# Optimization experiments

Hardware: AMD Instinct MI355X
Metric: run time of the kernel (lower is better)

The kernel has to match this reference:

```python
import jax, jax.numpy as jnp
import numpy as np

B, T = 4, 8
H, W = 120, 160
NON_SEM = 4
CAT = 16
MAP_CH = NON_SEM + CAT          # 20 map channels
FEAT_CH = 2 * NON_SEM + CAT     # 24 feature channels
RES = 5.0                       # cm per map cell
GLOBAL_M, LOCAL_M = 960, 240    # map_size/resolution, and /downscale
M2 = LOCAL_M * LOCAL_M
HFOV = 79.0
CAM_H_CM = 88.0
VISION_CM = 100 * RES           # vision_range cells -> cm
AGENT_R2 = 2.0 ** 2
EXPLORE_R2 = 3.0 ** 2
FX = W / (2.0 * float(np.tan(np.deg2rad(HFOV) / 2.0)))
FY = FX
CX, CY = W / 2.0, H / 2.0

LOCAL_POSE0 = jnp.array([LOCAL_M * RES / 2, LOCAL_M * RES / 2, 0.0], jnp.float32)
GLOBAL_POSE0 = jnp.array([GLOBAL_M * RES / 2, GLOBAL_M * RES / 2, 0.0], jnp.float32)
OFF = (GLOBAL_M - LOCAL_M) // 2
BOUNDS0 = jnp.array([OFF, OFF + LOCAL_M, OFF, OFF + LOCAL_M], jnp.int32)
ORIGINS0 = jnp.array([OFF * RES, OFF * RES, 0.0], jnp.float32)


def _splat1(flat, w):  # scatter-add scalar weights into the flattened local grid
    return jnp.zeros((M2,), jnp.float32).at[flat].add(w)


def _splatC(flat, vals):  # vals [C, N] -> [C, M2]
    return jnp.zeros((vals.shape[0], M2), jnp.float32).at[:, flat].add(vals)


def _step(carry, xs):
    lmap, gmap, lpose, gpose, bounds, origins = carry
    obs, delta, cam_T, done, upd = xs
    doneb = done != 0
    # per-env reset on episode end (init_map_and_pose_for_env)
    lmap = jnp.where(doneb[:, None, None, None], 0.0, lmap)
    gmap = jnp.where(doneb[:, None, None, None], 0.0, gmap)
    lpose = jnp.where(doneb[:, None], LOCAL_POSE0, lpose)
    gpose = jnp.where(doneb[:, None], GLOBAL_POSE0, gpose)
    bounds = jnp.where(doneb[:, None], BOUNDS0, bounds)
    origins = jnp.where(doneb[:, None], ORIGINS0, origins)

    # dead-reckoning pose update (delta in agent frame)
    th = jnp.deg2rad(lpose[:, 2])
    dx = delta[:, 0] * jnp.cos(th) - delta[:, 1] * jnp.sin(th)
    dy = delta[:, 0] * jnp.sin(th) + delta[:, 1] * jnp.cos(th)
    lpose = lpose + jnp.stack([dx, dy, delta[:, 2]], -1)

    # depth -> camera-frame point cloud (cm)
    depth = obs[:, 3] * 400.0 + 50.0  # [B,H,W]
    sem = obs[:, NON_SEM:]            # [B,CAT,H,W]
    uu = (jnp.arange(W, dtype=jnp.float32) - CX)[None, None, :]
    vv = (CY - jnp.arange(H, dtype=jnp.float32))[None, :, None]
    pts = jnp.stack([uu * depth / FX, vv * depth / FY, depth, jnp.ones_like(depth)], -1)
    pts = jnp.einsum('bij,bhwj->bhwi', cam_T, pts)  # camera extrinsics
    x_f, y_l, z_u = pts[..., 2], -pts[..., 0], pts[..., 1] + CAM_H_CM

    # agent frame -> local map frame
    th2 = jnp.deg2rad(lpose[:, 2])[:, None, None]
    wx = lpose[:, 0][:, None, None] + x_f * jnp.cos(th2) - y_l * jnp.sin(th2)
    wy = lpose[:, 1][:, None, None] + x_f * jnp.sin(th2) + y_l * jnp.cos(th2)
    ix = jnp.floor(wx / RES).astype(jnp.int32)
    iy = jnp.floor(wy / RES).astype(jnp.int32)
    valid = (depth > 25.0) & (depth < VISION_CM) & (ix >= 0) & (ix < LOCAL_M) & (iy >= 0) & (iy < LOCAL_M)
    flat = (jnp.clip(iy, 0, LOCAL_M - 1) * LOCAL_M + jnp.clip(ix, 0, LOCAL_M - 1)).reshape(B, -1)
    vm = valid.reshape(B, -1).astype(jnp.float32)
    obst_w = vm * ((z_u > 25.0) & (z_u < 150.0)).reshape(B, -1).astype(jnp.float32)

    exp_grid = jax.vmap(_splat1)(flat, vm).reshape(B, LOCAL_M, LOCAL_M)
    obst_grid = jax.vmap(_splat1)(flat, obst_w).reshape(B, LOCAL_M, LOCAL_M)
    sem_grid = jax.vmap(_splatC)(flat, sem.reshape(B, CAT, -1) * vm[:, None, :]).reshape(B, CAT, LOCAL_M, LOCAL_M)

    # agent location / been-close disks
    g = jnp.arange(LOCAL_M, dtype=jnp.float32)
    dxg = g[None, None, :] - (lpose[:, 0] / RES)[:, None, None]
    dyg = g[None, :, None] - (lpose[:, 1] / RES)[:, None, None]
    d2 = dxg * dxg + dyg * dyg
    agent = (d2 <= AGENT_R2).astype(jnp.float32)
    close = (d2 <= EXPLORE_R2).astype(jnp.float32)

    lmap = jnp.concatenate([
        jnp.maximum(lmap[:, 0], jnp.clip(obst_grid, 0.0, 1.0))[:, None],
        jnp.maximum(lmap[:, 1], jnp.clip(exp_grid, 0.0, 1.0))[:, None],
        agent[:, None],
        jnp.maximum(lmap[:, 3], close)[:, None],
        jnp.maximum(lmap[:, NON_SEM:], jnp.clip(sem_grid, 0.0, 1.0)),
    ], axis=1)

    # fuse local window into global map for envs flagged for update
    y1, x1 = bounds[:, 0], bounds[:, 2]
    crop = jax.vmap(lambda gm, y, x: jax.lax.dynamic_slice(gm, (0, y, x), (MAP_CH, LOCAL_M, LOCAL_M)))(gmap, y1, x1)
    updb = (upd != 0)[:, None, None, None]
    fused = jnp.where(updb, jnp.maximum(crop, lmap), crop)
    gmap = jax.vmap(lambda gm, c, y, x: jax.lax.dynamic_update_slice(gm, c, (0, y, x)))(gmap, fused, y1, x1)
    gpose = jnp.where((upd != 0)[:, None], lpose + origins, gpose)

    feats = jnp.concatenate([lmap[:, :NON_SEM], fused[:, :NON_SEM], lmap[:, NON_SEM:]], axis=1)
    return (lmap, gmap, lpose, gpose, bounds, origins), (feats, lpose, gpose, bounds, origins)


def _forward(obs_seq, pose_delta, cam_poses, init_local_map, init_global_map,
             init_local_pose, init_global_pose, init_origins,
             done_flags, update_flags, init_bounds):
    xs = (obs_seq.swapaxes(0, 1), pose_delta.swapaxes(0, 1), cam_poses.swapaxes(0, 1),
          done_flags.swapaxes(0, 1), update_flags.swapaxes(0, 1))
    carry0 = (init_local_map, init_global_map, init_local_pose, init_global_pose, init_bounds, init_origins)
    carry, ys = jax.lax.scan(_step, carry0, xs)
    feats, lp, gp, bnds, orgs = ys
    return (feats.swapaxes(0, 1), carry[0], carry[1], lp.swapaxes(0, 1), gp.swapaxes(0, 1),
            bnds.swapaxes(0, 1), orgs.swapaxes(0, 1))


def setup_inputs() -> dict:
    key = jax.random.key(0)
    ks = jax.random.split(key, 5)
    obs_seq = jax.random.uniform(ks[0], (B, T, MAP_CH, H, W), jnp.float32)
    pose_delta = jax.random.normal(ks[1], (B, T, 3), jnp.float32) * jnp.array([10.0, 2.0, 5.0], jnp.float32)
    cam_poses = jnp.eye(4, dtype=jnp.float32)[None, None] + 0.02 * jax.random.normal(ks[2], (B, T, 4, 4), jnp.float32)
    done_flags = jax.random.randint(ks[3], (B, T), 0, 2, jnp.int32)
    update_flags = jax.random.randint(ks[4], (B, T), 0, 2, jnp.int32)
    return {
        'obs_seq': obs_seq,
        'pose_delta': pose_delta,
        'done_flags': done_flags,
        'update_flags': update_flags,
        'cam_poses': cam_poses,
        'init_local_map': jnp.zeros((B, MAP_CH, LOCAL_M, LOCAL_M), jnp.float32),
        'init_global_map': jnp.zeros((B, MAP_CH, GLOBAL_M, GLOBAL_M), jnp.float32),
        'init_local_pose': jnp.tile(LOCAL_POSE0[None], (B, 1)),
        'init_global_pose': jnp.tile(GLOBAL_POSE0[None], (B, 1)),
        'init_bounds': jnp.tile(BOUNDS0[None], (B, 1)),
        'init_origins': jnp.tile(ORIGINS0[None], (B, 1)),
    }


def reference(obs_seq, pose_delta, done_flags, update_flags, cam_poses,
              init_local_map, init_global_map, init_local_pose, init_global_pose,
              init_bounds, init_origins):
    return _forward(obs_seq, pose_delta, cam_poses, init_local_map, init_global_map,
                    init_local_pose, init_global_pose, init_origins,
                    done_flags, update_flags, init_bounds)
```

## Files before the change

### kernel.cpp

```cpp
#include <hip/hip_runtime.h>
#include <math.h>

#define Bn 4
#define Tn 8
#define Hn 120
#define Wn 160
#define HWn (Hn * Wn)
#define NON_SEMn 4
#define CATn 16
#define MAP_CHn 20
#define FEAT_CHn 24
#define LOCAL_Mn 240
#define GLOBAL_Mn 960
#define M2n (LOCAL_Mn * LOCAL_Mn)
#define TBMn (Tn * Bn * M2n)
#define Pn (Tn * Bn * HWn)
#define NTILE_SCAN 1800
#define UPD_BLKS ((Bn * M2n + 255) / 256)
#define PROJ_BLKS ((Pn + 255) / 256)
#define GMAP_BLKS ((Bn * MAP_CHn * GLOBAL_Mn * GLOBAL_Mn / 4 + 255) / 256)

#define DEG2RADf ((float)0.017453292519943295)

typedef float vf4 __attribute__((ext_vector_type(4)));

#define OUT_FEATS 0
#define OUT_LMAP  44236800
#define OUT_GMAP  48844800
#define OUT_LP    122572800
#define OUT_GP    122572896
#define OUT_BNDS  122572992
#define OUT_ORGS  122573120

#define WS_CNTR   96
#define WS_REC2   128
#define WS_BSUM   (WS_REC2 + 2 * TBMn)
#define WS_CELL   (WS_BSUM + 2048)
#define WS_RECB   (WS_CELL + Pn)

__device__ __forceinline__ void pose_upto(const float* __restrict__ pose_delta,
                                          const int* __restrict__ done_flags,
                                          const float* __restrict__ init_lpose,
                                          int b, int tt,
                                          float& lx, float& ly, float& lz) {
#pragma clang fp contract(off)
    lx = init_lpose[b * 3 + 0];
    ly = init_lpose[b * 3 + 1];
    lz = init_lpose[b * 3 + 2];
    for (int t = 0; t <= tt; t++) {
        if (done_flags[b * Tn + t]) { lx = 600.0f; ly = 600.0f; lz = 0.0f; }
        float th = lz * DEG2RADf;
        float c = cosf(th), s = sinf(th);
        float d0 = pose_delta[(b * Tn + t) * 3 + 0];
        float d1 = pose_delta[(b * Tn + t) * 3 + 1];
        float d2 = pose_delta[(b * Tn + t) * 3 + 2];
        lx = lx + (d0 * c - d1 * s);
        ly = ly + (d0 * s + d1 * c);
        lz = lz + d2;
    }
}

__global__ void __launch_bounds__(256)
proj_gmap_kernel(const float* __restrict__ obs,
                 const float* __restrict__ cam,
                 const float* __restrict__ pose_delta,
                 const int* __restrict__ done_flags,
                 const int* __restrict__ upd_flags,
                 const float* __restrict__ init_lpose,
                 const float* __restrict__ init_gpose,
                 const int* __restrict__ init_bounds,
                 const float* __restrict__ init_origins,
                 const float* __restrict__ init_gmap,
                 uint2* __restrict__ rec2,
                 int* __restrict__ cellid,
                 float* __restrict__ out_lp,
                 float* __restrict__ out_gp,
                 float* __restrict__ out_bnds,
                 float* __restrict__ out_orgs,
                 float* __restrict__ out_gmap,
                 float fx) {
#pragma clang fp contract(off)
    if (blockIdx.x >= PROJ_BLKS) {
        size_t i4 = (size_t)(blockIdx.x - PROJ_BLKS) * 256 + threadIdx.x;
        const size_t total4 = (size_t)Bn * MAP_CHn * GLOBAL_Mn * GLOBAL_Mn / 4;
        if (i4 >= total4) return;
        size_t f = i4 * 4;
        int gx = (int)(f % GLOBAL_Mn);
        size_t r = f / GLOBAL_Mn;
        int gy = (int)(r % GLOBAL_Mn);
        size_t bc = r / GLOBAL_Mn;
        int b = (int)(bc / MAP_CHn);
        int y1 = init_bounds[b * 4 + 0];
        int x1 = init_bounds[b * 4 + 2];
        if (gy >= y1 && gy < y1 + LOCAL_Mn && gx >= x1 && gx < x1 + LOCAL_Mn) return;
        bool anyd = false;
        for (int t = 0; t < Tn; t++) anyd |= (done_flags[b * Tn + t] != 0);
        vf4 v;
        if (anyd) {
            v = (vf4)(0.0f);
        } else {
            v = __builtin_nontemporal_load((const vf4*)(init_gmap + f));
        }
        __builtin_nontemporal_store(v, (vf4*)(out_gmap + f));
        return;
    }

    if (blockIdx.x == 0 && threadIdx.x < Bn) {
        int b = threadIdx.x;
        float lx = init_lpose[b * 3 + 0], ly = init_lpose[b * 3 + 1], lz = init_lpose[b * 3 + 2];
        float gx = init_gpose[b * 3 + 0], gy = init_gpose[b * 3 + 1], gz = init_gpose[b * 3 + 2];
        int b0 = init_bounds[b * 4 + 0], b1 = init_bounds[b * 4 + 1];
        int b2i = init_bounds[b * 4 + 2], b3 = init_bounds[b * 4 + 3];
        float ox = init_origins[b * 3 + 0], oy = init_origins[b * 3 + 1], oz = init_origins[b * 3 + 2];
        for (int t = 0; t < Tn; t++) {
            int done = done_flags[b * Tn + t];
            int upd  = upd_flags[b * Tn + t];
            if (done) {
                lx = 600.0f; ly = 600.0f; lz = 0.0f;
                gx = 2400.0f; gy = 2400.0f; gz = 0.0f;
                b0 = 360; b1 = 600; b2i = 360; b3 = 600;
                ox = 1800.0f; oy = 1800.0f; oz = 0.0f;
            }
            float th = lz * DEG2RADf;
            float c = cosf(th), sn = sinf(th);
            float d0 = pose_delta[(b * Tn + t) * 3 + 0];
            float d1 = pose_delta[(b * Tn + t) * 3 + 1];
            float d2 = pose_delta[(b * Tn + t) * 3 + 2];
            lx = lx + (d0 * c - d1 * sn);
            ly = ly + (d0 * sn + d1 * c);
            lz = lz + d2;
            if (upd) { gx = lx + ox; gy = ly + oy; gz = lz + oz; }
            out_lp[(b * Tn + t) * 3 + 0] = lx;
            out_lp[(b * Tn + t) * 3 + 1] = ly;
            out_lp[(b * Tn + t) * 3 + 2] = lz;
            out_gp[(b * Tn + t) * 3 + 0] = gx;
            out_gp[(b * Tn + t) * 3 + 1] = gy;
            out_gp[(b * Tn + t) * 3 + 2] = gz;
            out_bnds[(b * Tn + t) * 4 + 0] = (float)b0;
            out_bnds[(b * Tn + t) * 4 + 1] = (float)b1;
            out_bnds[(b * Tn + t) * 4 + 2] = (float)b2i;
            out_bnds[(b * Tn + t) * 4 + 3] = (float)b3;
            out_orgs[(b * Tn + t) * 3 + 0] = ox;
            out_orgs[(b * Tn + t) * 3 + 1] = oy;
            out_orgs[(b * Tn + t) * 3 + 2] = oz;
        }
    }

    int g = blockIdx.x * 256 + threadIdx.x;
    if (g >= Pn) return;
    int p = g % HWn;
    int tb = g / HWn;
    int b = tb % Bn;
    int t = tb / Bn;
    int h = p / Wn, w = p % Wn;
    const float* ob = obs + (size_t)((b * Tn + t) * MAP_CHn) * HWn;
    float depth = ob[3 * HWn + p] * 400.0f + 50.0f;
    float u = (float)w - 80.0f;
    float v = 60.0f - (float)h;
    float px = u * depth / fx;
    float py = v * depth / fx;
    float pz = depth;
    const float* Tm = cam + (size_t)(b * Tn + t) * 16;
    float X = ((Tm[0] * px + Tm[1] * py) + Tm[2] * pz) + Tm[3];
    float Y = ((Tm[4] * px + Tm[5] * py) + Tm[6] * pz) + Tm[7];
    float Z = ((Tm[8] * px + Tm[9] * py) + Tm[10] * pz) + Tm[11];
    float x_f = Z;
    float y_l = -X;
    float z_u = Y + 88.0f;
    float lx, ly, lz;
    pose_upto(pose_delta, done_flags, init_lpose, b, t, lx, ly, lz);
    float th2 = lz * DEG2RADf;
    float c2 = cosf(th2), s2 = sinf(th2);
    float wx = (lx + x_f * c2) - y_l * s2;
    float wy = (ly + x_f * s2) + y_l * c2;
    int ix = (int)floorf(wx / 5.0f);
    int iy = (int)floorf(wy / 5.0f);
    bool valid = (depth > 25.0f) && (depth < 500.0f) &&
                 (ix >= 0) && (ix < LOCAL_Mn) && (iy >= 0) && (iy < LOCAL_Mn);
    int cell = -1;
    if (valid) {
        cell = (t * Bn + b) * M2n + iy * LOCAL_Mn + ix;
        unsigned addv = 1u + ((z_u > 25.0f && z_u < 150.0f) ? 65536u : 0u);
        atomicAdd(&rec2[cell].x, addv);
    }
    cellid[g] = cell;
}

__global__ void scan1_kernel(uint2* __restrict__ rec2,
                             unsigned* __restrict__ bsum,
                             unsigned* __restrict__ cntr) {
    __shared__ unsigned s[256];
    int tid = threadIdx.x;
    int base = blockIdx.x * 1024 + tid * 4;
    unsigned v0 = rec2[base].x & 0xFFFFu, v1 = rec2[base + 1].x & 0xFFFFu;
    unsigned v2 = rec2[base + 2].x & 0xFFFFu, v3 = rec2[base + 3].x & 0xFFFFu;
    unsigned tsum = v0 + v1 + v2 + v3;
    s[tid] = tsum;
    __syncthreads();
    for (int d = 1; d < 256; d <<= 1) {
        unsigned a = (tid >= d) ? s[tid - d] : 0u;
        __syncthreads();
        s[tid] += a;
        __syncthreads();
    }
    unsigned excl = s[tid] - tsum;
    if (tid == 255) bsum[blockIdx.x] = atomicAdd(cntr, s[255]);
    rec2[base].y     = excl;
    rec2[base + 1].y = excl + v0;
    rec2[base + 2].y = excl + v0 + v1;
    rec2[base + 3].y = excl + v0 + v1 + v2;
}

__global__ void scatter_copy_kernel(const float* __restrict__ obs,
                                    const int* __restrict__ cellid,
                                    const unsigned* __restrict__ bsum,
                                    uint2* __restrict__ rec2,
                                    float* __restrict__ recb) {
    int g = blockIdx.x * blockDim.x + threadIdx.x;
    if (g >= Pn) return;
    int c = cellid[g];
    if (c < 0) return;
    int p = g % HWn;
    int tb = g / HWn;
    int b = tb % Bn;
    int t = tb / Bn;
    const float* ob = obs + (size_t)((b * Tn + t) * MAP_CHn) * HWn;
    vf4 r[4];
#pragma unroll
    for (int q = 0; q < 4; q++) {
        r[q].x = ob[(size_t)(NON_SEMn + 4 * q + 0) * HWn + p];
        r[q].y = ob[(size_t)(NON_SEMn + 4 * q + 1) * HWn + p];
        r[q].z = ob[(size_t)(NON_SEMn + 4 * q + 2) * HWn + p];
        r[q].w = ob[(size_t)(NON_SEMn + 4 * q + 3) * HWn + p];
    }
    unsigned pos = bsum[c >> 10] + atomicAdd(&rec2[c].y, 1u);
    vf4* rp = (vf4*)(recb + (size_t)pos * CATn);
#pragma unroll
    for (int q = 0; q < 4; q++)
        __builtin_nontemporal_store(r[q], rp + q);
}

__global__ void __launch_bounds__(256)
update_kernel(const uint2* __restrict__ rec2,
              const unsigned* __restrict__ bsum,
              const float* __restrict__ recb,
              const int* __restrict__ done_flags,
              const int* __restrict__ upd_flags,
              const float* __restrict__ pose_delta,
              const float* __restrict__ init_lpose,
              const float* __restrict__ init_lmap,
              const float* __restrict__ init_gmap,
              const int* __restrict__ init_bounds,
              float* __restrict__ out_feats,
              float* __restrict__ out_lmap,
              float* __restrict__ out_gmap) {
#pragma clang fp contract(off)
    int idx = blockIdx.x * blockDim.x + threadIdx.x;
    if (idx >= Bn * M2n) return;
    int b = idx / M2n, j = idx % M2n;
    int y = j / LOCAL_Mn, x = j % LOCAL_Mn;
    int y1 = init_bounds[b * 4 + 0];
    int x1 = init_bounds[b * 4 + 2];

    float lm[MAP_CHn], cr[MAP_CHn];
#pragma unroll
    for (int ch = 0; ch < MAP_CHn; ch++)
        lm[ch] = __builtin_nontemporal_load(init_lmap + ((size_t)(b * MAP_CHn + ch)) * M2n + j);
#pragma unroll
    for (int ch = 0; ch < MAP_CHn; ch++)
        cr[ch] = __builtin_nontemporal_load(
            init_gmap + ((size_t)(b * MAP_CHn + ch) * GLOBAL_Mn + (y1 + y)) * GLOBAL_Mn + (x1 + x));

    float lx = init_lpose[b * 3 + 0];
    float ly = init_lpose[b * 3 + 1];
    float lz = init_lpose[b * 3 + 2];

    for (int t = 0; t < Tn; t++) {
        int done = done_flags[b * Tn + t];
        int upd  = upd_flags[b * Tn + t];
        if (done) {
#pragma unroll
            for (int ch = 0; ch < MAP_CHn; ch++) { lm[ch] = 0.0f; cr[ch] = 0.0f; }
            lx = 600.0f; ly = 600.0f; lz = 0.0f;
        }
        {
            float th = lz * DEG2RADf;
            float c = cosf(th), sn = sinf(th);
            float d0 = pose_delta[(b * Tn + t) * 3 + 0];
            float d1 = pose_delta[(b * Tn + t) * 3 + 1];
            float d2p = pose_delta[(b * Tn + t) * 3 + 2];
            lx = lx + (d0 * c - d1 * sn);
            ly = ly + (d0 * sn + d1 * c);
            lz = lz + d2p;
        }
        float dxg = (float)x - lx / 5.0f;
        float dyg = (float)y - ly / 5.0f;
        float d2 = dxg * dxg + dyg * dyg;
        float agent = (d2 <= 4.0f) ? 1.0f : 0.0f;
        float close = (d2 <= 9.0f) ? 1.0f : 0.0f;

        int cell = (t * Bn + b) * M2n + j;
        uint2 rc = rec2[cell];
        unsigned n = rc.x & 0xFFFFu;
        lm[0] = fmaxf(lm[0], (rc.x >> 16) ? 1.0f : 0.0f);
        lm[1] = fmaxf(lm[1], n ? 1.0f : 0.0f);
        lm[2] = agent;
        lm[3] = fmaxf(lm[3], close);

        if (n) {
            unsigned st = bsum[cell >> 10] + rc.y - n;
            float sem[CATn];
#pragma unroll
            for (int c = 0; c < CATn; c++) sem[c] = 0.0f;
            const vf4* rp = (const vf4*)(recb + (size_t)st * CATn);
            for (unsigned k = 0; k < n; k++) {
                vf4 r0 = rp[0], r1 = rp[1], r2 = rp[2], r3 = rp[3];
                rp += 4;
                sem[0] += r0.x;  sem[1] += r0.y;  sem[2] += r0.z;  sem[3] += r0.w;
                sem[4] += r1.x;  sem[5] += r1.y;  sem[6] += r1.z;  sem[7] += r1.w;
                sem[8] += r2.x;  sem[9] += r2.y;  sem[10] += r2.z; sem[11] += r2.w;
                sem[12] += r3.x; sem[13] += r3.y; sem[14] += r3.z; sem[15] += r3.w;
            }
#pragma unroll
            for (int c = 0; c < CATn; c++)
                lm[NON_SEMn + c] = fmaxf(lm[NON_SEMn + c], fminf(fmaxf(sem[c], 0.0f), 1.0f));
        }
        if (upd) {
#pragma unroll
            for (int ch = 0; ch < MAP_CHn; ch++) cr[ch] = fmaxf(cr[ch], lm[ch]);
        }

        size_t fb = ((size_t)(b * Tn + t) * FEAT_CHn) * M2n + j;
#pragma unroll
        for (int ch = 0; ch < NON_SEMn; ch++)
            __builtin_nontemporal_store(lm[ch], out_feats + fb + (size_t)ch * M2n);
#pragma unroll
        for (int ch = 0; ch < NON_SEMn; ch++)
            __builtin_nontemporal_store(cr[ch], out_feats + fb + (size_t)(NON_SEMn + ch) * M2n);
#pragma unroll
        for (int c = 0; c < CATn; c++)
            __builtin_nontemporal_store(lm[NON_SEMn + c], out_feats + fb + (size_t)(2 * NON_SEMn + c) * M2n);
    }

#pragma unroll
    for (int ch = 0; ch < MAP_CHn; ch++)
        __builtin_nontemporal_store(lm[ch], out_lmap + ((size_t)(b * MAP_CHn + ch)) * M2n + j);
#pragma unroll
    for (int ch = 0; ch < MAP_CHn; ch++)
        __builtin_nontemporal_store(
            cr[ch], out_gmap + ((size_t)(b * MAP_CHn + ch) * GLOBAL_Mn + (y1 + y)) * GLOBAL_Mn + (x1 + x));
}

extern "C" void kernel_launch(void* const* d_in, const int* in_sizes, int n_in,
                              void* d_out, int out_size, void* d_ws, size_t ws_size,
                              hipStream_t stream) {
    const float* obs        = (const float*)d_in[0];
    const float* pose_delta = (const float*)d_in[1];
    const int*   done_flags = (const int*)d_in[2];
    const int*   upd_flags  = (const int*)d_in[3];
    const float* cam_poses  = (const float*)d_in[4];
    const float* init_lmap  = (const float*)d_in[5];
    const float* init_gmap  = (const float*)d_in[6];
    const float* init_lpose = (const float*)d_in[7];
    const float* init_gpose = (const float*)d_in[8];
    const int*   init_bnds  = (const int*)d_in[9];
    const float* init_orgs  = (const float*)d_in[10];

    float* out = (float*)d_out;
    float* ws  = (float*)d_ws;

    unsigned* cntr   = (unsigned*)(ws + WS_CNTR);
    uint2*    rec2   = (uint2*)(ws + WS_REC2);
    unsigned* bsum   = (unsigned*)(ws + WS_BSUM);
    int*      cellid = (int*)(ws + WS_CELL);
    float*    recb   = ws + WS_RECB;

    float fx = (float)(160.0 / (2.0 * tan(79.0 * M_PI / 180.0 / 2.0)));

    (void)hipMemsetAsync(ws + WS_CNTR, 0,
                         (size_t)(32 + 2 * TBMn) * sizeof(float), stream);

    proj_gmap_kernel<<<PROJ_BLKS + GMAP_BLKS, 256, 0, stream>>>(
        obs, cam_poses, pose_delta, done_flags, upd_flags,
        init_lpose, init_gpose, init_bnds, init_orgs, init_gmap,
        rec2, cellid,
        out + OUT_LP, out + OUT_GP, out + OUT_BNDS, out + OUT_ORGS,
        out + OUT_GMAP, fx);

    scan1_kernel<<<NTILE_SCAN, 256, 0, stream>>>(rec2, bsum, cntr);

    scatter_copy_kernel<<<PROJ_BLKS, 256, 0, stream>>>(
        obs, cellid, bsum, rec2, recb);

    update_kernel<<<UPD_BLKS, 256, 0, stream>>>(
        rec2, bsum, recb, done_flags, upd_flags, pose_delta, init_lpose,
        init_lmap, init_gmap, init_bnds,
        out + OUT_FEATS, out + OUT_LMAP, out + OUT_GMAP);
}
```

Baseline: 842.9 us.

## Split map update across two thread halves and fuse global-map copy into it

The per-cell update kernel now runs two threads per local-map cell, each handling a disjoint channel subset (12 and 8 channels), with per-step record offsets preloaded up front. The global-map outside-window copy moves from the projection kernel into the final update kernel, so the bandwidth-heavy copy runs alongside the update. Scatter-copy stores become ordinary stores instead of nontemporal ones, so the scattered records may stay cached for the update pass. The split doubles parallelism and cuts registers per thread, at the cost of reading the record counts twice and duplicating some index math.

```diff
diff --git a/kernel.cpp b/kernel.cpp
--- a/kernel.cpp
+++ b/kernel.cpp
@@ -13,11 +13,12 @@
 #define LOCAL_Mn 240
 #define GLOBAL_Mn 960
 #define M2n (LOCAL_Mn * LOCAL_Mn)
+#define BMn (Bn * M2n)
 #define TBMn (Tn * Bn * M2n)
 #define Pn (Tn * Bn * HWn)
 #define NTILE_SCAN 1800
-#define UPD_BLKS ((Bn * M2n + 255) / 256)
 #define PROJ_BLKS ((Pn + 255) / 256)
+#define UPD2_BLKS ((2 * BMn + 255) / 256)
 #define GMAP_BLKS ((Bn * MAP_CHn * GLOBAL_Mn * GLOBAL_Mn / 4 + 255) / 256)
 
 #define DEG2RADf ((float)0.017453292519943295)
@@ -61,50 +62,23 @@
 }
 
 __global__ void __launch_bounds__(256)
-proj_gmap_kernel(const float* __restrict__ obs,
-                 const float* __restrict__ cam,
-                 const float* __restrict__ pose_delta,
-                 const int* __restrict__ done_flags,
-                 const int* __restrict__ upd_flags,
-                 const float* __restrict__ init_lpose,
-                 const float* __restrict__ init_gpose,
-                 const int* __restrict__ init_bounds,
-                 const float* __restrict__ init_origins,
-                 const float* __restrict__ init_gmap,
-                 uint2* __restrict__ rec2,
-                 int* __restrict__ cellid,
-                 float* __restrict__ out_lp,
-                 float* __restrict__ out_gp,
-                 float* __restrict__ out_bnds,
-                 float* __restrict__ out_orgs,
-                 float* __restrict__ out_gmap,
-                 float fx) {
+project_kernel(const float* __restrict__ obs,
+               const float* __restrict__ cam,
+               const float* __restrict__ pose_delta,
+               const int* __restrict__ done_flags,
+               const int* __restrict__ upd_flags,
+               const float* __restrict__ init_lpose,
+               const float* __restrict__ init_gpose,
+               const int* __restrict__ init_bounds,
+               const float* __restrict__ init_origins,
+               uint2* __restrict__ rec2,
+               int* __restrict__ cellid,
+               float* __restrict__ out_lp,
+               float* __restrict__ out_gp,
+               float* __restrict__ out_bnds,
+               float* __restrict__ out_orgs,
+               float fx) {
 #pragma clang fp contract(off)
-    if (blockIdx.x >= PROJ_BLKS) {
-        size_t i4 = (size_t)(blockIdx.x - PROJ_BLKS) * 256 + threadIdx.x;
-        const size_t total4 = (size_t)Bn * MAP_CHn * GLOBAL_Mn * GLOBAL_Mn / 4;
-        if (i4 >= total4) return;
-        size_t f = i4 * 4;
-        int gx = (int)(f % GLOBAL_Mn);
-        size_t r = f / GLOBAL_Mn;
-        int gy = (int)(r % GLOBAL_Mn);
-        size_t bc = r / GLOBAL_Mn;
-        int b = (int)(bc / MAP_CHn);
-        int y1 = init_bounds[b * 4 + 0];
-        int x1 = init_bounds[b * 4 + 2];
-        if (gy >= y1 && gy < y1 + LOCAL_Mn && gx >= x1 && gx < x1 + LOCAL_Mn) return;
-        bool anyd = false;
-        for (int t = 0; t < Tn; t++) anyd |= (done_flags[b * Tn + t] != 0);
-        vf4 v;
-        if (anyd) {
-            v = (vf4)(0.0f);
-        } else {
-            v = __builtin_nontemporal_load((const vf4*)(init_gmap + f));
-        }
-        __builtin_nontemporal_store(v, (vf4*)(out_gmap + f));
-        return;
-    }
-
     if (blockIdx.x == 0 && threadIdx.x < Bn) {
         int b = threadIdx.x;
         float lx = init_lpose[b * 3 + 0], ly = init_lpose[b * 3 + 1], lz = init_lpose[b * 3 + 2];
@@ -236,54 +210,67 @@
     unsigned pos = bsum[c >> 10] + atomicAdd(&rec2[c].y, 1u);
     vf4* rp = (vf4*)(recb + (size_t)pos * CATn);
 #pragma unroll
-    for (int q = 0; q < 4; q++)
-        __builtin_nontemporal_store(r[q], rp + q);
-}
-
-__global__ void __launch_bounds__(256)
-update_kernel(const uint2* __restrict__ rec2,
-              const unsigned* __restrict__ bsum,
-              const float* __restrict__ recb,
-              const int* __restrict__ done_flags,
-              const int* __restrict__ upd_flags,
-              const float* __restrict__ pose_delta,
-              const float* __restrict__ init_lpose,
-              const float* __restrict__ init_lmap,
-              const float* __restrict__ init_gmap,
-              const int* __restrict__ init_bounds,
-              float* __restrict__ out_feats,
-              float* __restrict__ out_lmap,
-              float* __restrict__ out_gmap) {
+    for (int q = 0; q < 4; q++) rp[q] = r[q];
+}
+
+template <int Q>
+__device__ __forceinline__ void update_half(
+        int b, int j,
+        const uint2* __restrict__ rec2,
+        const unsigned* __restrict__ bsum,
+        const float* __restrict__ recb,
+        const int* __restrict__ done_flags,
+        const int* __restrict__ upd_flags,
+        const float* __restrict__ pose_delta,
+        const float* __restrict__ init_lpose,
+        const float* __restrict__ init_lmap,
+        const float* __restrict__ init_gmap,
+        int y1, int x1,
+        float* __restrict__ out_feats,
+        float* __restrict__ out_lmap,
+        float* __restrict__ out_gmap) {
 #pragma clang fp contract(off)
-    int idx = blockIdx.x * blockDim.x + threadIdx.x;
-    if (idx >= Bn * M2n) return;
-    int b = idx / M2n, j = idx % M2n;
+    constexpr int CH0 = Q ? 12 : 0;
+    constexpr int NCH = Q ? 8 : 12;
     int y = j / LOCAL_Mn, x = j % LOCAL_Mn;
-    int y1 = init_bounds[b * 4 + 0];
-    int x1 = init_bounds[b * 4 + 2];
-
-    float lm[MAP_CHn], cr[MAP_CHn];
-#pragma unroll
-    for (int ch = 0; ch < MAP_CHn; ch++)
-        lm[ch] = __builtin_nontemporal_load(init_lmap + ((size_t)(b * MAP_CHn + ch)) * M2n + j);
-#pragma unroll
-    for (int ch = 0; ch < MAP_CHn; ch++)
-        cr[ch] = __builtin_nontemporal_load(
-            init_gmap + ((size_t)(b * MAP_CHn + ch) * GLOBAL_Mn + (y1 + y)) * GLOBAL_Mn + (x1 + x));
-
-    float lx = init_lpose[b * 3 + 0];
-    float ly = init_lpose[b * 3 + 1];
-    float lz = init_lpose[b * 3 + 2];
+
+    float lm[NCH], cr[NCH];
+#pragma unroll
+    for (int i = 0; i < NCH; i++)
+        lm[i] = __builtin_nontemporal_load(init_lmap + ((size_t)(b * MAP_CHn + CH0 + i)) * M2n + j);
+#pragma unroll
+    for (int i = 0; i < NCH; i++)
+        cr[i] = __builtin_nontemporal_load(
+            init_gmap + ((size_t)(b * MAP_CHn + CH0 + i) * GLOBAL_Mn + (y1 + y)) * GLOBAL_Mn + (x1 + x));
+
+    uint2 rc8[Tn];
+#pragma unroll
+    for (int t = 0; t < Tn; t++) rc8[t] = rec2[(t * Bn + b) * M2n + j];
+    unsigned st8[Tn];
+#pragma unroll
+    for (int t = 0; t < Tn; t++) {
+        unsigned n = rc8[t].x & 0xFFFFu;
+        st8[t] = bsum[((t * Bn + b) * M2n + j) >> 10] + rc8[t].y - n;
+    }
+
+    float lx = 0.0f, ly = 0.0f, lz = 0.0f;
+    if (Q == 0) {
+        lx = init_lpose[b * 3 + 0];
+        ly = init_lpose[b * 3 + 1];
+        lz = init_lpose[b * 3 + 2];
+    }
 
     for (int t = 0; t < Tn; t++) {
         int done = done_flags[b * Tn + t];
         int upd  = upd_flags[b * Tn + t];
         if (done) {
 #pragma unroll
-            for (int ch = 0; ch < MAP_CHn; ch++) { lm[ch] = 0.0f; cr[ch] = 0.0f; }
-            lx = 600.0f; ly = 600.0f; lz = 0.0f;
-        }
-        {
+            for (int i = 0; i < NCH; i++) { lm[i] = 0.0f; cr[i] = 0.0f; }
+        }
+        unsigned n = rc8[t].x & 0xFFFFu;
+
+        if (Q == 0) {
+            if (done) { lx = 600.0f; ly = 600.0f; lz = 0.0f; }
             float th = lz * DEG2RADf;
             float c = cosf(th), sn = sinf(th);
             float d0 = pose_delta[(b * Tn + t) * 3 + 0];
@@ -292,63 +279,116 @@
             lx = lx + (d0 * c - d1 * sn);
             ly = ly + (d0 * sn + d1 * c);
             lz = lz + d2p;
-        }
-        float dxg = (float)x - lx / 5.0f;
-        float dyg = (float)y - ly / 5.0f;
-        float d2 = dxg * dxg + dyg * dyg;
-        float agent = (d2 <= 4.0f) ? 1.0f : 0.0f;
-        float close = (d2 <= 9.0f) ? 1.0f : 0.0f;
-
-        int cell = (t * Bn + b) * M2n + j;
-        uint2 rc = rec2[cell];
-        unsigned n = rc.x & 0xFFFFu;
-        lm[0] = fmaxf(lm[0], (rc.x >> 16) ? 1.0f : 0.0f);
-        lm[1] = fmaxf(lm[1], n ? 1.0f : 0.0f);
-        lm[2] = agent;
-        lm[3] = fmaxf(lm[3], close);
+            float dxg = (float)x - lx / 5.0f;
+            float dyg = (float)y - ly / 5.0f;
+            float d2 = dxg * dxg + dyg * dyg;
+            lm[0] = fmaxf(lm[0], (rc8[t].x >> 16) ? 1.0f : 0.0f);
+            lm[1] = fmaxf(lm[1], n ? 1.0f : 0.0f);
+            lm[2] = (d2 <= 4.0f) ? 1.0f : 0.0f;
+            lm[3] = fmaxf(lm[3], (d2 <= 9.0f) ? 1.0f : 0.0f);
+        }
 
         if (n) {
-            unsigned st = bsum[cell >> 10] + rc.y - n;
-            float sem[CATn];
-#pragma unroll
-            for (int c = 0; c < CATn; c++) sem[c] = 0.0f;
-            const vf4* rp = (const vf4*)(recb + (size_t)st * CATn);
+            float sem[8];
+#pragma unroll
+            for (int c = 0; c < 8; c++) sem[c] = 0.0f;
+            const vf4* rp = (const vf4*)(recb + (size_t)st8[t] * CATn) + (Q ? 2 : 0);
             for (unsigned k = 0; k < n; k++) {
-                vf4 r0 = rp[0], r1 = rp[1], r2 = rp[2], r3 = rp[3];
+                vf4 ra = rp[0], rb = rp[1];
                 rp += 4;
-                sem[0] += r0.x;  sem[1] += r0.y;  sem[2] += r0.z;  sem[3] += r0.w;
-                sem[4] += r1.x;  sem[5] += r1.y;  sem[6] += r1.z;  sem[7] += r1.w;
-                sem[8] += r2.x;  sem[9] += r2.y;  sem[10] += r2.z; sem[11] += r2.w;
-                sem[12] += r3.x; sem[13] += r3.y; sem[14] += r3.z; sem[15] += r3.w;
+                sem[0] += ra.x; sem[1] += ra.y; sem[2] += ra.z; sem[3] += ra.w;
+                sem[4] += rb.x; sem[5] += rb.y; sem[6] += rb.z; sem[7] += rb.w;
             }
-#pragma unroll
-            for (int c = 0; c < CATn; c++)
-                lm[NON_SEMn + c] = fmaxf(lm[NON_SEMn + c], fminf(fmaxf(sem[c], 0.0f), 1.0f));
+            constexpr int L0 = Q ? 0 : 4;
+#pragma unroll
+            for (int c = 0; c < 8; c++)
+                lm[L0 + c] = fmaxf(lm[L0 + c], fminf(fmaxf(sem[c], 0.0f), 1.0f));
         }
         if (upd) {
 #pragma unroll
-            for (int ch = 0; ch < MAP_CHn; ch++) cr[ch] = fmaxf(cr[ch], lm[ch]);
+            for (int i = 0; i < NCH; i++) cr[i] = fmaxf(cr[i], lm[i]);
         }
 
         size_t fb = ((size_t)(b * Tn + t) * FEAT_CHn) * M2n + j;
-#pragma unroll
-        for (int ch = 0; ch < NON_SEMn; ch++)
-            __builtin_nontemporal_store(lm[ch], out_feats + fb + (size_t)ch * M2n);
-#pragma unroll
-        for (int ch = 0; ch < NON_SEMn; ch++)
-            __builtin_nontemporal_store(cr[ch], out_feats + fb + (size_t)(NON_SEMn + ch) * M2n);
-#pragma unroll
-        for (int c = 0; c < CATn; c++)
-            __builtin_nontemporal_store(lm[NON_SEMn + c], out_feats + fb + (size_t)(2 * NON_SEMn + c) * M2n);
-    }
-
-#pragma unroll
-    for (int ch = 0; ch < MAP_CHn; ch++)
-        __builtin_nontemporal_store(lm[ch], out_lmap + ((size_t)(b * MAP_CHn + ch)) * M2n + j);
-#pragma unroll
-    for (int ch = 0; ch < MAP_CHn; ch++)
+        if (Q == 0) {
+#pragma unroll
+            for (int i = 0; i < 4; i++)
+                __builtin_nontemporal_store(lm[i], out_feats + fb + (size_t)i * M2n);
+#pragma unroll
+            for (int i = 0; i < 4; i++)
+                __builtin_nontemporal_store(cr[i], out_feats + fb + (size_t)(4 + i) * M2n);
+#pragma unroll
+            for (int i = 0; i < 8; i++)
+                __builtin_nontemporal_store(lm[4 + i], out_feats + fb + (size_t)(8 + i) * M2n);
+        } else {
+#pragma unroll
+            for (int i = 0; i < 8; i++)
+                __builtin_nontemporal_store(lm[i], out_feats + fb + (size_t)(16 + i) * M2n);
+        }
+    }
+
+#pragma unroll
+    for (int i = 0; i < NCH; i++)
+        __builtin_nontemporal_store(lm[i], out_lmap + ((size_t)(b * MAP_CHn + CH0 + i)) * M2n + j);
+#pragma unroll
+    for (int i = 0; i < NCH; i++)
         __builtin_nontemporal_store(
-            cr[ch], out_gmap + ((size_t)(b * MAP_CHn + ch) * GLOBAL_Mn + (y1 + y)) * GLOBAL_Mn + (x1 + x));
+            cr[i], out_gmap + ((size_t)(b * MAP_CHn + CH0 + i) * GLOBAL_Mn + (y1 + y)) * GLOBAL_Mn + (x1 + x));
+}
+
+__global__ void __launch_bounds__(256)
+mega_kernel(const uint2* __restrict__ rec2,
+            const unsigned* __restrict__ bsum,
+            const float* __restrict__ recb,
+            const int* __restrict__ done_flags,
+            const int* __restrict__ upd_flags,
+            const float* __restrict__ pose_delta,
+            const float* __restrict__ init_lpose,
+            const float* __restrict__ init_lmap,
+            const float* __restrict__ init_gmap,
+            const int* __restrict__ init_bounds,
+            float* __restrict__ out_feats,
+            float* __restrict__ out_lmap,
+            float* __restrict__ out_gmap) {
+    if (blockIdx.x >= UPD2_BLKS) {
+        size_t i4 = (size_t)(blockIdx.x - UPD2_BLKS) * 256 + threadIdx.x;
+        const size_t total4 = (size_t)Bn * MAP_CHn * GLOBAL_Mn * GLOBAL_Mn / 4;
+        if (i4 >= total4) return;
+        size_t f = i4 * 4;
+        int gx = (int)(f % GLOBAL_Mn);
+        size_t r = f / GLOBAL_Mn;
+        int gy = (int)(r % GLOBAL_Mn);
+        size_t bc = r / GLOBAL_Mn;
+        int b = (int)(bc / MAP_CHn);
+        int y1 = init_bounds[b * 4 + 0];
+        int x1 = init_bounds[b * 4 + 2];
+        if (gy >= y1 && gy < y1 + LOCAL_Mn && gx >= x1 && gx < x1 + LOCAL_Mn) return;
+        bool anyd = false;
+        for (int t = 0; t < Tn; t++) anyd |= (done_flags[b * Tn + t] != 0);
+        vf4 v;
+        if (anyd) {
+            v = (vf4)(0.0f);
+        } else {
+            v = __builtin_nontemporal_load((const vf4*)(init_gmap + f));
+        }
+        __builtin_nontemporal_store(v, (vf4*)(out_gmap + f));
+        return;
+    }
+
+    int idx = blockIdx.x * 256 + threadIdx.x;
+    int q = idx / BMn;
+    int cid = idx - q * BMn;
+    int b = cid / M2n, j = cid % M2n;
+    int y1 = init_bounds[b * 4 + 0];
+    int x1 = init_bounds[b * 4 + 2];
+    if (q == 0)
+        update_half<0>(b, j, rec2, bsum, recb, done_flags, upd_flags,
+                       pose_delta, init_lpose, init_lmap, init_gmap,
+                       y1, x1, out_feats, out_lmap, out_gmap);
+    else
+        update_half<1>(b, j, rec2, bsum, recb, done_flags, upd_flags,
+                       pose_delta, init_lpose, init_lmap, init_gmap,
+                       y1, x1, out_feats, out_lmap, out_gmap);
 }
 
 extern "C" void kernel_launch(void* const* d_in, const int* in_sizes, int n_in,
@@ -380,19 +420,18 @@
     (void)hipMemsetAsync(ws + WS_CNTR, 0,
                          (size_t)(32 + 2 * TBMn) * sizeof(float), stream);
 
-    proj_gmap_kernel<<<PROJ_BLKS + GMAP_BLKS, 256, 0, stream>>>(
+    project_kernel<<<PROJ_BLKS, 256, 0, stream>>>(
         obs, cam_poses, pose_delta, done_flags, upd_flags,
-        init_lpose, init_gpose, init_bnds, init_orgs, init_gmap,
+        init_lpose, init_gpose, init_bnds, init_orgs,
         rec2, cellid,
-        out + OUT_LP, out + OUT_GP, out + OUT_BNDS, out + OUT_ORGS,
-        out + OUT_GMAP, fx);
+        out + OUT_LP, out + OUT_GP, out + OUT_BNDS, out + OUT_ORGS, fx);
 
     scan1_kernel<<<NTILE_SCAN, 256, 0, stream>>>(rec2, bsum, cntr);
 
     scatter_copy_kernel<<<PROJ_BLKS, 256, 0, stream>>>(
         obs, cellid, bsum, rec2, recb);
 
-    update_kernel<<<UPD_BLKS, 256, 0, stream>>>(
+    mega_kernel<<<UPD2_BLKS + GMAP_BLKS, 256, 0, stream>>>(
         rec2, bsum, recb, done_flags, upd_flags, pose_delta, init_lpose,
         init_lmap, init_gmap, init_bnds,
         out + OUT_FEATS, out + OUT_LMAP, out + OUT_GMAP);
```

New measurement: 792.4 us. 1.06x faster.
